# Kernel tuning notes

Measured on AMD Instinct MI355X. Metric: run time of the kernel, lower is better.

The kernel has to match this reference:

```python
import jax, jax.numpy as jnp
import numpy as np

B, M, C, IMG, P, D, L, H, DFF, NC = 16, 4, 3, 224, 16, 768, 12, 12, 3072, 1000
G = IMG // P
S = G * G + 1
HD = D // H
EPS = 1e-6
SCALE = HD ** -0.5


def setup_inputs() -> dict:
    key = jax.random.key(0)
    ks = jax.random.split(key, 12)
    w = lambda k, shape: (jax.random.normal(k, shape) * 0.02).astype(jnp.float32)
    return {
        'x': jax.random.normal(ks[0], (B, C, IMG, IMG), jnp.float32),
        'x_tangent': jax.random.normal(ks[1], (B, M, C, IMG, IMG), jnp.float32),
        'patch_w': w(ks[2], (D, C * P * P)), 'patch_b': jnp.zeros((D,), jnp.float32),
        'cls_token': w(ks[3], (1, 1, D)), 'pos_embed': w(ks[4], (1, S, D)),
        'ln1_g': jnp.ones((L, D), jnp.float32), 'ln1_b': jnp.zeros((L, D), jnp.float32),
        'qkv_w': w(ks[5], (L, 3 * D, D)), 'qkv_b': jnp.zeros((L, 3 * D), jnp.float32),
        'proj_w': w(ks[6], (L, D, D)), 'proj_b': jnp.zeros((L, D), jnp.float32),
        'ln2_g': jnp.ones((L, D), jnp.float32), 'ln2_b': jnp.zeros((L, D), jnp.float32),
        'fc1_w': w(ks[7], (L, DFF, D)), 'fc1_b': jnp.zeros((L, DFF), jnp.float32),
        'fc2_w': w(ks[8], (L, D, DFF)), 'fc2_b': jnp.zeros((L, D), jnp.float32),
        'normf_g': jnp.ones((D,), jnp.float32), 'normf_b': jnp.zeros((D,), jnp.float32),
        'head_w': w(ks[9], (NC, D)), 'head_b': jnp.zeros((NC,), jnp.float32),
    }


def _patchify(img):
    # [b,C,IMG,IMG] -> [b, G*G, C*P*P], matching Conv2d(patch) weight layout (c, ph, pw)
    b = img.shape[0]
    p = img.reshape(b, C, G, P, G, P).transpose(0, 2, 4, 1, 3, 5)
    return p.reshape(b, G * G, C * P * P)


def _ln_jvp(x, t, g, b):
    # x: [B,S,D], t: [B,M,S,D]; params constant w.r.t. tangent directions
    mu = x.mean(-1, keepdims=True)
    xc = x - mu
    inv = jax.lax.rsqrt((xc * xc).mean(-1, keepdims=True) + EPS)
    xh = xc * inv
    y = xh * g + b
    xh_b, inv_b = xh[:, None], inv[:, None]
    ty = g * inv_b * (t - t.mean(-1, keepdims=True) - xh_b * (xh_b * t).mean(-1, keepdims=True))
    return y, ty


def _gelu_jvp(x, t):
    # exact (erf) GELU and its derivative; x: [B,S,F], t: [B,M,S,F]
    cdf = 0.5 * (1.0 + jax.lax.erf(x * 0.7071067811865476))
    pdf = jnp.exp(-0.5 * x * x) * 0.3989422804014327
    return x * cdf, t * (cdf + x * pdf)[:, None]


def _softmax_jvp(s, ts):
    # s: [B,H,S,S], ts: [B,M,H,S,S]
    a = jax.nn.softmax(s, axis=-1)
    a_b = a[:, None]
    ta = a_b * (ts - (a_b * ts).sum(-1, keepdims=True))
    return a, ta


def reference(x, x_tangent, patch_w, patch_b, cls_token, pos_embed,
              ln1_g, ln1_b, qkv_w, qkv_b, proj_w, proj_b, ln2_g, ln2_b,
              fc1_w, fc1_b, fc2_w, fc2_b, normf_g, normf_b, head_w, head_b):
    # patch embed (primal + tangent; bias/pos/cls are constants -> zero tangent)
    h = _patchify(x) @ patch_w.T + patch_b                                  # [B,N,D]
    th = (_patchify(x_tangent.reshape(B * M, C, IMG, IMG)) @ patch_w.T).reshape(B, M, G * G, D)
    cls = jnp.broadcast_to(cls_token, (B, 1, D))
    h = jnp.concatenate([cls, h], axis=1) + pos_embed                       # [B,S,D]
    th = jnp.concatenate([jnp.zeros((B, M, 1, D), th.dtype), th], axis=2)   # [B,M,S,D]

    for l in range(L):
        # --- attention (manual JVP, matching the torch einsum path) ---
        y, ty = _ln_jvp(h, th, ln1_g[l], ln1_b[l])
        qkv = y @ qkv_w[l].T + qkv_b[l]
        tqkv = ty @ qkv_w[l].T
        q, k, v = jnp.split(qkv, 3, axis=-1)
        tq, tk, tv = jnp.split(tqkv, 3, axis=-1)
        q = q.reshape(B, S, H, HD); k = k.reshape(B, S, H, HD); v = v.reshape(B, S, H, HD)
        tq = tq.reshape(B, M, S, H, HD); tk = tk.reshape(B, M, S, H, HD); tv = tv.reshape(B, M, S, H, HD)
        s = jnp.einsum('bqhd,bkhd->bhqk', q, k) * SCALE
        ts = (jnp.einsum('bmqhd,bkhd->bmhqk', tq, k)
              + jnp.einsum('bqhd,bmkhd->bmhqk', q, tk)) * SCALE
        a, ta = _softmax_jvp(s, ts)
        o = jnp.einsum('bhqk,bkhd->bqhd', a, v).reshape(B, S, D)
        to = (jnp.einsum('bmhqk,bkhd->bmqhd', ta, v)
              + jnp.einsum('bhqk,bmkhd->bmqhd', a, tv)).reshape(B, M, S, D)
        h = h + o @ proj_w[l].T + proj_b[l]
        th = th + to @ proj_w[l].T
        # --- mlp ---
        y, ty = _ln_jvp(h, th, ln2_g[l], ln2_b[l])
        y = y @ fc1_w[l].T + fc1_b[l]
        ty = ty @ fc1_w[l].T
        y, ty = _gelu_jvp(y, ty)
        h = h + y @ fc2_w[l].T + fc2_b[l]
        th = th + ty @ fc2_w[l].T

    y, ty = _ln_jvp(h, th, normf_g, normf_b)
    logits = y[:, 0] @ head_w.T + head_b            # token pooling
    tlogits = ty[:, :, 0] @ head_w.T                 # [B,M,NC]
    return logits, tlogits
```

## Files before the change

kernel.cpp:

```cpp
#include <hip/hip_runtime.h>
#include <hip/hip_bf16.h>

#define DEVI __device__ __forceinline__

typedef short  bf16x8 __attribute__((ext_vector_type(8)));
typedef float  f32x4  __attribute__((ext_vector_type(4)));

static constexpr int BB   = 16;
static constexpr int MM   = 4;
static constexpr int CC   = 3;
static constexpr int IMG  = 224;
static constexpr int PPP  = 16;
static constexpr int DD   = 768;
static constexpr int LL   = 12;
static constexpr int HH   = 12;
static constexpr int DFF  = 3072;
static constexpr int NCLS = 1000;
static constexpr int GG   = 14;
static constexpr int SS   = 197;
static constexpr int HD   = 64;
static constexpr int BT   = BB*SS;
static constexpr int BMT  = BB*MM*SS;
static constexpr int RT   = BT+BMT;
static constexpr int RP   = 15872;
static constexpr int SP   = 208;
static constexpr int LDP  = 216;
static constexpr int QLD  = 3*DD;
static constexpr int PRP  = BB*GG*GG;
static constexpr int PRT  = (BB+BB*MM)*GG*GG;
static constexpr float EPSV  = 1e-6f;
static constexpr float SCALE = 0.125f;

static constexpr int NQW  = QLD*DD;
static constexpr int NPW  = DD*DD;
static constexpr int NF1W = DFF*DD;
static constexpr int NF2W = DD*DFF;
static constexpr int WTOT = NQW+NPW+NF1W+NF2W;

DEVI unsigned short f2bf(float x){
  union { float f; unsigned u; } v; v.f = x;
  unsigned r = v.u + 0x7fffu + ((v.u>>16)&1u);
  return (unsigned short)(r>>16);
}
DEVI float bf2f(unsigned short x){
  union { unsigned u; float f; } v; v.u = ((unsigned)x)<<16;
  return v.f;
}
DEVI f32x4 mfma16(bf16x8 a, bf16x8 b, f32x4 c){
  return __builtin_amdgcn_mfma_f32_16x16x32_bf16(a,b,c,0,0,0);
}
typedef const void __attribute__((address_space(1)))* gas1;
typedef void __attribute__((address_space(3)))* las3;


DEVI bf16x8 cvt8(const float* src){
  float4 a = *(const float4*)src;
  float4 b = *(const float4*)(src+4);
  bf16x8 o;
  o[0]=(short)f2bf(a.x); o[1]=(short)f2bf(a.y); o[2]=(short)f2bf(a.z); o[3]=(short)f2bf(a.w);
  o[4]=(short)f2bf(b.x); o[5]=(short)f2bf(b.y); o[6]=(short)f2bf(b.z); o[7]=(short)f2bf(b.w);
  return o;
}

__global__ __launch_bounds__(256) void f2bf8_kernel(const float* __restrict__ in,
    unsigned short* __restrict__ out, size_t n8){
  size_t i = (size_t)blockIdx.x*256 + threadIdx.x;
  if (i < n8) *(bf16x8*)(out + i*8) = cvt8(in + i*8);
}

__global__ __launch_bounds__(256) void conv_all_v(const float* __restrict__ qkvw,
    const float* __restrict__ projw, const float* __restrict__ f1w,
    const float* __restrict__ f2w, unsigned short* __restrict__ wl){
  int l = blockIdx.y;
  size_t i = ((size_t)blockIdx.x*256 + threadIdx.x)*8;
  const float* src;
  if (i < NQW)                src = qkvw + (size_t)l*NQW + i;
  else if (i < NQW+NPW)       src = projw + (size_t)l*NPW + (i-NQW);
  else if (i < NQW+NPW+NF1W)  src = f1w + (size_t)l*NF1W + (i-NQW-NPW);
  else                        src = f2w + (size_t)l*NF2W + (i-NQW-NPW-NF1W);
  *(bf16x8*)(wl + (size_t)l*WTOT + i) = cvt8(src);
}

__global__ __launch_bounds__(256) void conv_layer_v(const float* __restrict__ qkvw,
    const float* __restrict__ projw, const float* __restrict__ f1w,
    const float* __restrict__ f2w, unsigned short* __restrict__ wl){
  size_t i = ((size_t)blockIdx.x*256 + threadIdx.x)*8;
  const float* src;
  if (i < NQW)                src = qkvw + i;
  else if (i < NQW+NPW)       src = projw + (i-NQW);
  else if (i < NQW+NPW+NF1W)  src = f1w + (i-NQW-NPW);
  else                        src = f2w + (i-NQW-NPW-NF1W);
  *(bf16x8*)(wl + i) = cvt8(src);
}

__global__ __launch_bounds__(256) void init_h(float* __restrict__ hh,
    const float* __restrict__ cls, const float* __restrict__ pos,
    const float* __restrict__ patch_b){
  size_t i = (size_t)blockIdx.x*256 + threadIdx.x;
  int r = (int)(i/DD), c = (int)(i%DD);
  float v = 0.f;
  if (r < BT){
    int s_ = r % SS;
    v = pos[(size_t)s_*DD + c] + (s_==0 ? cls[c] : patch_b[c]);
  }
  hh[i] = v;
}

__global__ __launch_bounds__(256) void patchify_k(const float* __restrict__ x,
    const float* __restrict__ xt, unsigned short* __restrict__ pat){
  size_t i = (size_t)blockIdx.x*256 + threadIdx.x;
  int r = (int)(i/DD), kk = (int)(i%DD);
  int c = kk>>8, rem = kk&255, py = rem>>4, px = rem&15;
  const float* src;
  if (r < PRP){
    int b_ = r/(GG*GG), p = r%(GG*GG);
    src = x + (((size_t)b_*CC + c)*IMG + (size_t)(p/GG)*PPP + py)*IMG + (p%GG)*PPP + px;
  } else {
    int rr = r-PRP; int bm = rr/(GG*GG), p = rr%(GG*GG);
    src = xt + (((size_t)bm*CC + c)*IMG + (size_t)(p/GG)*PPP + py)*IMG + (p%GG)*PPP + px;
  }
  pat[i] = f2bf(*src);
}


DEVI void blockSum4(float&a,float&b,float&c,float&d,float* red){
  #pragma unroll
  for (int off=32; off; off>>=1){
    a += __shfl_xor(a,off,64); b += __shfl_xor(b,off,64);
    c += __shfl_xor(c,off,64); d += __shfl_xor(d,off,64);
  }
  int w = threadIdx.x>>6;
  if ((threadIdx.x&63)==0){ red[w]=a; red[4+w]=b; red[8+w]=c; red[12+w]=d; }
  __syncthreads();
  a = red[0]+red[1]+red[2]+red[3];
  b = red[4]+red[5]+red[6]+red[7];
  c = red[8]+red[9]+red[10]+red[11];
  d = red[12]+red[13]+red[14]+red[15];
  __syncthreads();
}

__global__ __launch_bounds__(256) void ln_group(const float* __restrict__ hh,
    const float* __restrict__ g, const float* __restrict__ bb,
    unsigned short* __restrict__ ybf){
  __shared__ float red[4][10];
  int r = blockIdx.x;
  int b_ = r/SS, s_ = r%SS;
  int t = threadIdx.x;
  const float* xx = hh + (size_t)r*DD;
  float x0=xx[t], x1=xx[t+256], x2=xx[t+512];
  size_t trow[4];
  float tv[4][3];
  #pragma unroll
  for (int m=0;m<4;m++){
    trow[m] = (size_t)BT + ((size_t)(b_*MM+m))*SS + s_;
    const float* tt = hh + trow[m]*DD;
    tv[m][0]=tt[t]; tv[m][1]=tt[t+256]; tv[m][2]=tt[t+512];
  }
  float s[10];
  s[0]=x0+x1+x2; s[1]=x0*x0+x1*x1+x2*x2;
  #pragma unroll
  for (int m=0;m<4;m++){
    s[2+2*m]=tv[m][0]+tv[m][1]+tv[m][2];
    s[3+2*m]=x0*tv[m][0]+x1*tv[m][1]+x2*tv[m][2];
  }
  #pragma unroll
  for (int k=0;k<10;k++){
    float v = s[k];
    #pragma unroll
    for (int off=32; off; off>>=1) v += __shfl_xor(v, off, 64);
    s[k] = v;
  }
  int w = t>>6;
  if ((t&63)==0){
    #pragma unroll
    for (int k=0;k<10;k++) red[w][k]=s[k];
  }
  __syncthreads();
  #pragma unroll
  for (int k=0;k<10;k++) s[k] = red[0][k]+red[1][k]+red[2][k]+red[3][k];
  float mu  = s[0]*(1.f/DD);
  float inv = rsqrtf(s[1]*(1.f/DD) - mu*mu + EPSV);
  float g0=g[t], g1=g[t+256], g2=g[t+512];
  float h0=(x0-mu)*inv, h1=(x1-mu)*inv, h2=(x2-mu)*inv;
  {
    unsigned short* y = ybf + (size_t)r*DD;
    y[t]     = f2bf(h0*g0 + bb[t]);
    y[t+256] = f2bf(h1*g1 + bb[t+256]);
    y[t+512] = f2bf(h2*g2 + bb[t+512]);
  }
  #pragma unroll
  for (int m=0;m<4;m++){
    float tmean = s[2+2*m]*(1.f/DD);
    float dot   = inv*(s[3+2*m]*(1.f/DD) - mu*tmean);
    unsigned short* y = ybf + trow[m]*DD;
    y[t]     = f2bf(g0*inv*(tv[m][0] - tmean - h0*dot));
    y[t+256] = f2bf(g1*inv*(tv[m][1] - tmean - h1*dot));
    y[t+512] = f2bf(g2*inv*(tv[m][2] - tmean - h2*dot));
  }
}

__global__ __launch_bounds__(256) void ln_head(const float* __restrict__ hh,
    const float* __restrict__ g, const float* __restrict__ bb,
    unsigned short* __restrict__ ybf){
  __shared__ float red[16];
  int ri = blockIdx.x;
  int t = threadIdx.x;
  if (ri < BB){
    size_t row = (size_t)ri*SS;
    const float* x = hh + row*DD;
    float x0=x[t], x1=x[t+256], x2=x[t+512];
    float s1=x0+x1+x2, s2=x0*x0+x1*x1+x2*x2, s3=0.f, s4=0.f;
    blockSum4(s1,s2,s3,s4,red);
    float mu  = s1*(1.f/DD);
    float inv = rsqrtf(s2*(1.f/DD) - mu*mu + EPSV);
    unsigned short* y = ybf + row*DD;
    y[t]     = f2bf((x0-mu)*inv*g[t]     + bb[t]);
    y[t+256] = f2bf((x1-mu)*inv*g[t+256] + bb[t+256]);
    y[t+512] = f2bf((x2-mu)*inv*g[t+512] + bb[t+512]);
  } else {
    int t2 = ri - BB;
    size_t row = (size_t)BT + (size_t)t2*SS;
    size_t prow = (size_t)(t2/MM)*SS;
    const float* tt = hh + row*DD;
    const float* xx = hh + prow*DD;
    float t0=tt[t], t1=tt[t+256], t2v=tt[t+512];
    float x0=xx[t], x1=xx[t+256], x2=xx[t+512];
    float s1=x0+x1+x2, s2=x0*x0+x1*x1+x2*x2;
    float s3=t0+t1+t2v, s4=x0*t0+x1*t1+x2*t2v;
    blockSum4(s1,s2,s3,s4,red);
    float mu  = s1*(1.f/DD);
    float inv = rsqrtf(s2*(1.f/DD) - mu*mu + EPSV);
    float tmean = s3*(1.f/DD);
    float dot   = inv*(s4*(1.f/DD) - mu*tmean);
    unsigned short* y = ybf + row*DD;
    y[t]     = f2bf(g[t]    *inv*(t0  - tmean - (x0-mu)*inv*dot));
    y[t+256] = f2bf(g[t+256]*inv*(t1  - tmean - (x1-mu)*inv*dot));
    y[t+512] = f2bf(g[t+512]*inv*(t2v - tmean - (x2-mu)*inv*dot));
  }
}


template<int MODE>
__global__ __launch_bounds__(256,2) void gemm_bt(
    const unsigned short* __restrict__ A,
    const unsigned short* __restrict__ Aalt, int asplit, int lda,
    const unsigned short* __restrict__ W, int K, int N, int Mrows,
    float* __restrict__ outf, unsigned short* __restrict__ outb, int ldc,
    const float* __restrict__ bias, int bias_limit)
{
  __shared__ __attribute__((aligned(16))) unsigned short As[128*64];
  __shared__ __attribute__((aligned(16))) unsigned short Bs[128*64];
  const int tid = threadIdx.x;
  const int wave = tid>>6, lane = tid&63;
  const int tM = blockIdx.y, tN = blockIdx.x;
  f32x4 acc[4][4];
  f32x4 zf = {0.f,0.f,0.f,0.f};
  #pragma unroll
  for (int m=0;m<4;m++)
    #pragma unroll
    for (int n=0;n<4;n++) acc[m][n] = zf;
  const int wm = wave>>1, wn = wave&1;
  const int lrow = lane&15, lk8 = (lane>>4)<<3;
  const int srow = tid>>3;
  const int scol = (tid&7)<<3;
  const size_t arow0 = (size_t)tM*128;
  const size_t brow0 = (size_t)tN*128;

  for (int k0=0; k0<K; k0+=64){
    #pragma unroll
    for (int i=0;i<4;i++){
      int row = (int)arow0 + srow + i*32;
      const unsigned short* abase = (row < asplit) ? Aalt : A;
      const unsigned short* ga = abase + (size_t)row*lda + (k0+scol);
      __builtin_amdgcn_global_load_lds((gas1)ga, (las3)(As + i*2048 + wave*512), 16, 0, 0);
      const unsigned short* gb = W + (brow0+srow+i*32)*(size_t)K + (k0+scol);
      __builtin_amdgcn_global_load_lds((gas1)gb, (las3)(Bs + i*2048 + wave*512), 16, 0, 0);
    }
    __syncthreads();
    #pragma unroll
    for (int kk=0; kk<64; kk+=32){
      bf16x8 af[4], bw[4];
      #pragma unroll
      for (int m=0;m<4;m++) af[m] = *(const bf16x8*)(As + (wm*64+m*16+lrow)*64 + kk+lk8);
      #pragma unroll
      for (int n=0;n<4;n++) bw[n] = *(const bf16x8*)(Bs + (wn*64+n*16+lrow)*64 + kk+lk8);
      #pragma unroll
      for (int m=0;m<4;m++)
        #pragma unroll
        for (int n=0;n<4;n++)
          acc[m][n] = mfma16(af[m], bw[n], acc[m][n]);
    }
    __syncthreads();
  }

  const int colbase = tN*128 + wn*64 + lrow;
  const int rowbase = tM*128 + wm*64 + ((lane>>4)<<2);
  #pragma unroll
  for (int n=0;n<4;n++){
    int col = colbase + n*16;
    #pragma unroll
    for (int m=0;m<4;m++){
      #pragma unroll
      for (int i=0;i<4;i++){
        int r = rowbase + m*16 + i;
        float v = acc[m][n][i];
        if (MODE==0){
          if (r < bias_limit) v += bias[col];
          outb[(size_t)r*ldc + col] = f2bf(v);
        } else if (MODE==1){
          if (r < Mrows){
            if (r < bias_limit) v += bias[col];
            outf[(size_t)r*ldc + col] += v;
          }
        } else {
          if (r < PRT){
            int orow;
            if (r < PRP) orow = (r/196)*197 + 1 + r%196;
            else { int rr = r-PRP; orow = BT + (rr/196)*197 + 1 + rr%196; }
            outf[(size_t)orow*ldc + col] += v;
          }
        }
      }
    }
  }
}

__global__ __launch_bounds__(256) void transpose_v(const unsigned short* __restrict__ qkv,
    unsigned short* __restrict__ vT, unsigned short* __restrict__ tvT){
  __shared__ unsigned short tile[SP*65];
  int inst = blockIdx.x;
  size_t rowbase; unsigned short* dst; int h;
  if (inst < BB*HH){ int b_=inst/HH; h=inst%HH; rowbase=(size_t)b_*SS; dst = vT + (size_t)inst*HD*SP; }
  else { int i2=inst-BB*HH; int bm=i2/HH; h=i2%HH; rowbase=(size_t)BT+(size_t)bm*SS; dst = tvT + (size_t)i2*HD*SP; }
  int coff = 2*DD + h*HD;
  for (int i=threadIdx.x; i<SP*HD; i+=256){
    int k = i>>6, d = i&63;
    unsigned short v = (k<SS) ? qkv[(rowbase+k)*QLD + coff + d] : (unsigned short)0;
    tile[k*65+d] = v;
  }
  __syncthreads();
  for (int i=threadIdx.x; i<HD*SP; i+=256){
    int d = i/SP, k = i%SP;
    dst[(size_t)d*SP + k] = tile[k*65+d];
  }
}

__global__ __launch_bounds__(256) void attn_s1_pv(const unsigned short* __restrict__ qkv,
    unsigned short* __restrict__ abf, const unsigned short* __restrict__ vT,
    unsigned short* __restrict__ obf){
  __shared__ __attribute__((aligned(16))) unsigned short pa[64*LDP];
  int qt = blockIdx.x, inst = blockIdx.y;
  int wave = threadIdx.x>>6, lane = threadIdx.x&63;
  int lrow = lane&15, lk = (lane>>4)<<3;
  int q0 = qt*64 + wave*16;
  f32x4 acc[13];
  f32x4 zf = {0.f,0.f,0.f,0.f};
  #pragma unroll
  for (int n=0;n<13;n++) acc[n]=zf;
  int h = inst % HH, b_ = inst / HH;
  size_t prow = (size_t)b_*SS;
  const unsigned short* Ab = qkv + (prow + q0 + lrow)*QLD + h*HD + lk;
  const unsigned short* Bb = qkv + prow*QLD + DD + h*HD + lk;
  #pragma unroll
  for (int kk=0; kk<HD; kk+=32){
    bf16x8 av = *(const bf16x8*)(Ab + kk);
    #pragma unroll
    for (int n=0;n<13;n++){
      bf16x8 bv = *(const bf16x8*)(Bb + (size_t)(n*16+lrow)*QLD + kk);
      acc[n] = mfma16(av, bv, acc[n]);
    }
  }
  int grp = lane>>4;
  unsigned short* obase = abf + (size_t)inst*SP*SP;
  bool okc12 = (lrow < 5);
  #pragma unroll
  for (int i=0;i<4;i++){
    int qr = q0 + grp*4 + i;
    float val[13], e[13];
    float mv = -1e30f;
    #pragma unroll
    for (int n=0;n<13;n++){
      val[n] = acc[n][i]*SCALE;
      if (n<12 || okc12) mv = fmaxf(mv, val[n]);
    }
    #pragma unroll
    for (int off=8; off; off>>=1) mv = fmaxf(mv, __shfl_xor(mv, off, 64));
    float s = 0.f;
    #pragma unroll
    for (int n=0;n<13;n++){
      e[n] = (n<12 || okc12) ? __expf(val[n]-mv) : 0.f;
      s += e[n];
    }
    #pragma unroll
    for (int off=8; off; off>>=1) s += __shfl_xor(s, off, 64);
    float inv = 1.f/s;
    unsigned short* lrp = pa + (size_t)(wave*16 + grp*4 + i)*LDP;
    unsigned short* orow = obase + (size_t)qr*SP;
    #pragma unroll
    for (int n=0;n<13;n++){
      unsigned short pv_ = f2bf(e[n]*inv);
      lrp[n*16+lrow] = pv_;
      if (qr < SS) orow[n*16+lrow] = pv_;
    }
  }
  __syncthreads();
  f32x4 pacc[4];
  #pragma unroll
  for (int n=0;n<4;n++) pacc[n]=zf;
  const unsigned short* Vb = vT + (size_t)inst*HD*SP;
  const unsigned short* Arow = pa + (size_t)(wave*16 + lrow)*LDP;
  #pragma unroll
  for (int ks=0; ks<6; ks++){
    int kb = ks*32 + lk;
    bf16x8 av = *(const bf16x8*)(Arow + kb);
    #pragma unroll
    for (int n=0;n<4;n++){
      bf16x8 bv = *(const bf16x8*)(Vb + (size_t)(n*16+lrow)*SP + kb);
      pacc[n] = mfma16(av, bv, pacc[n]);
    }
  }
  {
    int kb = 192 + lk;
    const bf16x8 ZV = {0,0,0,0,0,0,0,0};
    bool ok = (lk < 16);
    bf16x8 av = ok ? *(const bf16x8*)(Arow + kb) : ZV;
    #pragma unroll
    for (int n=0;n<4;n++){
      bf16x8 bv = ok ? *(const bf16x8*)(Vb + (size_t)(n*16+lrow)*SP + kb) : ZV;
      pacc[n] = mfma16(av, bv, pacc[n]);
    }
  }
  size_t orow0 = (size_t)b_*SS;
  int qr0 = q0 + (grp<<2);
  #pragma unroll
  for (int n=0;n<4;n++){
    int cc = h*HD + n*16 + lrow;
    #pragma unroll
    for (int i=0;i<4;i++){
      int qr = qr0 + i;
      if (qr < SS) obf[(orow0+qr)*DD + cc] = f2bf(pacc[n][i]);
    }
  }
}

__global__ __launch_bounds__(256) void attn_s2_pv(const unsigned short* __restrict__ qkv,
    const unsigned short* __restrict__ abf, const unsigned short* __restrict__ vT,
    const unsigned short* __restrict__ tvT, unsigned short* __restrict__ obf){
  __shared__ __attribute__((aligned(16))) unsigned short sa[64*LDP];
  __shared__ __attribute__((aligned(16))) unsigned short ta[64*LDP];
  int qt = blockIdx.x, il = blockIdx.y;
  int wave = threadIdx.x>>6, lane = threadIdx.x&63;
  int lrow = lane&15, lk = (lane>>4)<<3;
  int q0 = qt*64 + wave*16;
  int h = il % HH;
  int bmix = il / HH;
  int b_ = bmix / MM;
  int bh = b_*HH + h;
  {
    const unsigned short* abase = abf + (size_t)bh*SP*SP;
    int qb = qt*64;
    for (int c = threadIdx.x; c < 64*26; c += 256){
      int rl = c/26, c8 = (c%26)*8;
      int qr = qb + rl; if (qr > SS-1) qr = SS-1;
      *(bf16x8*)(sa + (size_t)rl*LDP + c8) = *(const bf16x8*)(abase + (size_t)qr*SP + c8);
    }
  }
  f32x4 acc[13];
  f32x4 zf = {0.f,0.f,0.f,0.f};
  #pragma unroll
  for (int n=0;n<13;n++) acc[n]=zf;
  size_t prow = (size_t)b_*SS;
  size_t trow = (size_t)BT + (size_t)bmix*SS;
  #pragma unroll
  for (int p=0;p<2;p++){
    size_t ar = (p==0) ? trow : prow;
    size_t br = (p==1) ? trow : prow;
    const unsigned short* Ab = qkv + (ar + q0 + lrow)*QLD + h*HD + lk;
    const unsigned short* Bb = qkv + br*QLD + DD + h*HD + lk;
    #pragma unroll
    for (int kk=0; kk<HD; kk+=32){
      bf16x8 av = *(const bf16x8*)(Ab + kk);
      #pragma unroll
      for (int n=0;n<13;n++){
        bf16x8 bv = *(const bf16x8*)(Bb + (size_t)(n*16+lrow)*QLD + kk);
        acc[n] = mfma16(av, bv, acc[n]);
      }
    }
  }
  __syncthreads();
  int grp = lane>>4;
  #pragma unroll
  for (int i=0;i<4;i++){
    int rl = wave*16 + grp*4 + i;
    const unsigned short* arow = sa + (size_t)rl*LDP;
    float av[13], tv[13];
    float dot = 0.f;
    #pragma unroll
    for (int n=0;n<13;n++){
      tv[n] = acc[n][i]*SCALE;
      av[n] = bf2f(arow[n*16+lrow]);
      dot += av[n]*tv[n];
    }
    #pragma unroll
    for (int off=8; off; off>>=1) dot += __shfl_xor(dot, off, 64);
    unsigned short* trp = ta + (size_t)rl*LDP;
    #pragma unroll
    for (int n=0;n<13;n++) trp[n*16+lrow] = f2bf(av[n]*(tv[n]-dot));
  }
  __syncthreads();
  f32x4 pacc[4];
  #pragma unroll
  for (int n=0;n<4;n++) pacc[n]=zf;
  #pragma unroll
  for (int p=0;p<2;p++){
    const unsigned short* Arow = (p==0 ? ta : sa) + (size_t)(wave*16 + lrow)*LDP;
    const unsigned short* Bb = (p==0) ? vT + (size_t)bh*HD*SP
                                      : tvT + (size_t)il*HD*SP;
    #pragma unroll
    for (int ks=0; ks<6; ks++){
      int kb = ks*32 + lk;
      bf16x8 av = *(const bf16x8*)(Arow + kb);
      #pragma unroll
      for (int n=0;n<4;n++){
        bf16x8 bv = *(const bf16x8*)(Bb + (size_t)(n*16+lrow)*SP + kb);
        pacc[n] = mfma16(av, bv, pacc[n]);
      }
    }
    {
      int kb = 192 + lk;
      const bf16x8 ZV = {0,0,0,0,0,0,0,0};
      bool ok = (lk < 16);
      bf16x8 av = ok ? *(const bf16x8*)(Arow + kb) : ZV;
      #pragma unroll
      for (int n=0;n<4;n++){
        bf16x8 bv = ok ? *(const bf16x8*)(Bb + (size_t)(n*16+lrow)*SP + kb) : ZV;
        pacc[n] = mfma16(av, bv, pacc[n]);
      }
    }
  }
  size_t orow0 = (size_t)BT + (size_t)bmix*SS;
  int qr0 = q0 + (grp<<2);
  #pragma unroll
  for (int n=0;n<4;n++){
    int cc = h*HD + n*16 + lrow;
    #pragma unroll
    for (int i=0;i<4;i++){
      int qr = qr0 + i;
      if (qr < SS) obf[(orow0+qr)*DD + cc] = f2bf(pacc[n][i]);
    }
  }
}

__global__ __launch_bounds__(256) void gelu_group(unsigned short* __restrict__ fc1o,
                                                  unsigned short* __restrict__ pgbf){
  int r = blockIdx.x;
  int b_ = r/SS, s_ = r%SS;
  const bf16x8* pb = (const bf16x8*)(fc1o + (size_t)r*DFF);
  bf16x8* pg = (bf16x8*)(pgbf + (size_t)r*DFF);
  bf16x8* tb[4];
  #pragma unroll
  for (int m=0;m<4;m++)
    tb[m] = (bf16x8*)(fc1o + ((size_t)BT + (size_t)(b_*MM+m)*SS + s_)*DFF);
  for (int c = threadIdx.x; c < DFF/8; c += 256){
    bf16x8 xv = pb[c];
    float deriv[8];
    bf16x8 o;
    #pragma unroll
    for (int j=0;j<8;j++){
      float x = bf2f((unsigned short)xv[j]);
      float cdf = 0.5f*(1.f + erff(x*0.70710678118654752f));
      float pdf = __expf(-0.5f*x*x)*0.39894228040143267f;
      o[j] = (short)f2bf(x*cdf);
      deriv[j] = cdf + x*pdf;
    }
    pg[c] = o;
    #pragma unroll
    for (int m=0;m<4;m++){
      bf16x8 tv8 = tb[m][c];
      bf16x8 w;
      #pragma unroll
      for (int j=0;j<8;j++) w[j] = (short)f2bf(bf2f((unsigned short)tv8[j])*deriv[j]);
      tb[m][c] = w;
    }
  }
}

__global__ __launch_bounds__(256) void head_k(const unsigned short* __restrict__ ybf,
    const float* __restrict__ hw, const float* __restrict__ hb, float* __restrict__ out){
  __shared__ float ysh[DD];
  int ri = blockIdx.x;
  size_t yrow; float* o; bool wb;
  if (ri < BB){ yrow = (size_t)ri*SS; o = out + (size_t)ri*NCLS; wb = true; }
  else { int t2 = ri-BB; yrow = (size_t)BT + (size_t)t2*SS; o = out + (size_t)BB*NCLS + (size_t)t2*NCLS; wb = false; }
  for (int d=threadIdx.x; d<DD; d+=256) ysh[d] = bf2f(ybf[yrow*DD + d]);
  __syncthreads();
  for (int n=threadIdx.x; n<NCLS; n+=256){
    const float* wrow = hw + (size_t)n*DD;
    float acc = wb ? hb[n] : 0.f;
    for (int d=0; d<DD; d++) acc += ysh[d]*wrow[d];
    o[n] = acc;
  }
}

extern "C" void kernel_launch(void* const* d_in, const int* in_sizes, int n_in,
                              void* d_out, int out_size, void* d_ws, size_t ws_size,
                              hipStream_t stream)
{
  const float* x      = (const float*)d_in[0];
  const float* xt     = (const float*)d_in[1];
  const float* patch_w= (const float*)d_in[2];
  const float* patch_b= (const float*)d_in[3];
  const float* cls    = (const float*)d_in[4];
  const float* pos    = (const float*)d_in[5];
  const float* ln1_g  = (const float*)d_in[6];
  const float* ln1_b  = (const float*)d_in[7];
  const float* qkv_w  = (const float*)d_in[8];
  const float* qkv_b  = (const float*)d_in[9];
  const float* proj_w = (const float*)d_in[10];
  const float* proj_b = (const float*)d_in[11];
  const float* ln2_g  = (const float*)d_in[12];
  const float* ln2_b  = (const float*)d_in[13];
  const float* fc1_w  = (const float*)d_in[14];
  const float* fc1_b  = (const float*)d_in[15];
  const float* fc2_w  = (const float*)d_in[16];
  const float* fc2_b  = (const float*)d_in[17];
  const float* nf_g   = (const float*)d_in[18];
  const float* nf_b   = (const float*)d_in[19];
  const float* head_w = (const float*)d_in[20];
  const float* head_b = (const float*)d_in[21];
  float* out = (float*)d_out;

  char* ws = (char*)d_ws;
  size_t off = 0;
  auto alloc = [&](size_t bytes)->char*{
    char* p = ws + off;
    off = (off + bytes + 255) & ~(size_t)255;
    return p;
  };

  unsigned short *w_patch, *wl, *ybf, *qkvbf, *vT, *tvT, *abf, *fc1o, *pgbf;
  float *hh;
  auto layout = [&](bool allw)->size_t{
    off = 0;
    w_patch = (unsigned short*)alloc((size_t)DD*DD*2);
    wl      = (unsigned short*)alloc((size_t)WTOT*2*(allw?LL:1));
    hh      = (float*)alloc((size_t)RP*DD*4);
    ybf     = (unsigned short*)alloc((size_t)RP*DD*2);
    size_t slab0 = off;
    qkvbf = (unsigned short*)alloc((size_t)RP*QLD*2);
    vT    = (unsigned short*)alloc((size_t)BB*HH*HD*SP*2);
    tvT   = (unsigned short*)alloc((size_t)BB*MM*HH*HD*SP*2);
    abf   = (unsigned short*)alloc((size_t)BB*HH*SP*SP*2);
    size_t endA = off;
    off = slab0;
    fc1o = (unsigned short*)alloc((size_t)RP*DFF*2);
    pgbf = (unsigned short*)alloc((size_t)BT*DFF*2);
    size_t endB = off;
    return (endA > endB) ? endA : endB;
  };

  bool allw = true;
  size_t need = layout(true);
  if (need > ws_size){ need = layout(false); allw = false; }
  if (need > ws_size){
    (void)hipMemsetAsync(d_out, 0x7f, (size_t)out_size*4, stream);
    return;
  }

  dim3 blk(256);
  f2bf8_kernel<<<dim3((DD*DD/8+255)/256), blk, 0, stream>>>(patch_w, w_patch, (size_t)DD*DD/8);
  if (allw)
    conv_all_v<<<dim3(WTOT/8/256, LL), blk, 0, stream>>>(qkv_w, proj_w, fc1_w, fc2_w, wl);
  init_h<<<dim3((RP*DD)/256), blk, 0, stream>>>(hh, cls, pos, patch_b);
  patchify_k<<<dim3((PRT*DD)/256), blk, 0, stream>>>(x, xt, ybf);
  gemm_bt<2><<<dim3(DD/128, 123), blk, 0, stream>>>(ybf, nullptr, 0, DD, w_patch, DD, DD, PRT,
                                                    hh, nullptr, DD, nullptr, 0);

  for (int l=0; l<LL; l++){
    if (!allw)
      conv_layer_v<<<dim3(WTOT/8/256), blk, 0, stream>>>(qkv_w+(size_t)l*NQW, proj_w+(size_t)l*NPW,
                                                         fc1_w+(size_t)l*NF1W, fc2_w+(size_t)l*NF2W, wl);
    const unsigned short* w_qkv = wl + (allw ? (size_t)l*WTOT : 0);
    const unsigned short* w_proj= w_qkv + NQW;
    const unsigned short* w_fc1 = w_qkv + NQW + NPW;
    const unsigned short* w_fc2 = w_qkv + NQW + NPW + NF1W;

    ln_group<<<dim3(BT), blk, 0, stream>>>(hh, ln1_g+(size_t)l*DD, ln1_b+(size_t)l*DD, ybf);
    gemm_bt<0><<<dim3(QLD/128, RP/128), blk, 0, stream>>>(ybf, nullptr, 0, DD, w_qkv,
        DD, QLD, RT, nullptr, qkvbf, QLD, qkv_b+(size_t)l*QLD, BT);
    transpose_v<<<dim3(BB*HH + BB*MM*HH), blk, 0, stream>>>(qkvbf, vT, tvT);
    attn_s1_pv<<<dim3(4, BB*HH), blk, 0, stream>>>(qkvbf, abf, vT, ybf);
    attn_s2_pv<<<dim3(4, BB*MM*HH), blk, 0, stream>>>(qkvbf, abf, vT, tvT, ybf);
    gemm_bt<1><<<dim3(DD/128, RP/128), blk, 0, stream>>>(ybf, nullptr, 0, DD, w_proj,
        DD, DD, RT, hh, nullptr, DD, proj_b+(size_t)l*DD, BT);
    ln_group<<<dim3(BT), blk, 0, stream>>>(hh, ln2_g+(size_t)l*DD, ln2_b+(size_t)l*DD, ybf);
    gemm_bt<0><<<dim3(DFF/128, RP/128), blk, 0, stream>>>(ybf, nullptr, 0, DD, w_fc1,
        DD, DFF, RT, nullptr, fc1o, DFF, fc1_b+(size_t)l*DFF, BT);
    gelu_group<<<dim3(BT), blk, 0, stream>>>(fc1o, pgbf);
    gemm_bt<1><<<dim3(DD/128, RP/128), blk, 0, stream>>>(fc1o, pgbf, BT, DFF, w_fc2,
        DFF, DD, RT, hh, nullptr, DD, fc2_b+(size_t)l*DD, BT);
  }

  ln_head<<<dim3(BB + BB*MM), blk, 0, stream>>>(hh, nf_g, nf_b, ybf);
  head_k<<<dim3(BB + BB*MM), blk, 0, stream>>>(ybf, head_w, head_b, out);
}
```

Baseline: 7.476 ms.

## Use 256x256 double-buffered GEMM with swizzled LDS and 8 waves

Replaces the 128x128 single-buffered bf16 GEMM with a 256x256 tile kernel using 512 threads (8 waves, each computing 128x64). It double-buffers the LDS stages so the next K-tile's global-to-LDS load overlaps the current MFMAs, and removes one barrier per iteration. It also XOR-swizzles the LDS column slots to avoid bank conflicts and raises wave priority around the MFMA block. The larger tile cuts operand re-fetch per FLOP. The cost is 128KB of LDS per block, which may allow only one block per CU, plus fewer blocks overall (e.g. 3x62 for the D-wide GEMMs) and higher register pressure from 32 accumulators.

Measured after the change: 9.096 ms. 1.22x slower.

```diff
diff --git a/kernel.cpp b/kernel.cpp
--- a/kernel.cpp
+++ b/kernel.cpp
@@ -241,65 +241,100 @@
 
 
 template<int MODE>
-__global__ __launch_bounds__(256,2) void gemm_bt(
+__global__ __launch_bounds__(512,2) void gemm_bt8(
     const unsigned short* __restrict__ A,
     const unsigned short* __restrict__ Aalt, int asplit, int lda,
     const unsigned short* __restrict__ W, int K, int N, int Mrows,
     float* __restrict__ outf, unsigned short* __restrict__ outb, int ldc,
     const float* __restrict__ bias, int bias_limit)
 {
-  __shared__ __attribute__((aligned(16))) unsigned short As[128*64];
-  __shared__ __attribute__((aligned(16))) unsigned short Bs[128*64];
+  __shared__ __attribute__((aligned(16))) unsigned short As[2][256*64];
+  __shared__ __attribute__((aligned(16))) unsigned short Bs[2][256*64];
   const int tid = threadIdx.x;
-  const int wave = tid>>6, lane = tid&63;
+  const int lane = tid&63;
+  const int wave = tid>>6;
   const int tM = blockIdx.y, tN = blockIdx.x;
-  f32x4 acc[4][4];
+  const int wm = wave>>2, wn = wave&3;
+  const int lrow = lane&15;
+  const int lslot = lane>>4;
+  const int srow8 = tid>>3;
+  const int sslot = tid&7;
+
+  f32x4 acc[8][4];
   f32x4 zf = {0.f,0.f,0.f,0.f};
   #pragma unroll
-  for (int m=0;m<4;m++)
+  for (int m=0;m<8;m++)
     #pragma unroll
     for (int n=0;n<4;n++) acc[m][n] = zf;
-  const int wm = wave>>1, wn = wave&1;
-  const int lrow = lane&15, lk8 = (lane>>4)<<3;
-  const int srow = tid>>3;
-  const int scol = (tid&7)<<3;
-  const size_t arow0 = (size_t)tM*128;
-  const size_t brow0 = (size_t)tN*128;
-
-  for (int k0=0; k0<K; k0+=64){
-    #pragma unroll
-    for (int i=0;i<4;i++){
-      int row = (int)arow0 + srow + i*32;
-      const unsigned short* abase = (row < asplit) ? Aalt : A;
-      const unsigned short* ga = abase + (size_t)row*lda + (k0+scol);
-      __builtin_amdgcn_global_load_lds((gas1)ga, (las3)(As + i*2048 + wave*512), 16, 0, 0);
-      const unsigned short* gb = W + (brow0+srow+i*32)*(size_t)K + (k0+scol);
-      __builtin_amdgcn_global_load_lds((gas1)gb, (las3)(Bs + i*2048 + wave*512), 16, 0, 0);
+
+  const int nk = K>>6;
+
+  auto stage = [&](int kt, int b){
+    const int k0 = kt<<6;
+    #pragma unroll
+    for (int c=0;c<4;c++){
+      int rD = c*64 + srow8;
+      int gcol = k0 + ((sslot ^ (rD&7))<<3);
+      int grow = tM*256 + rD;
+      const unsigned short* ab = (grow < asplit) ? Aalt : A;
+      __builtin_amdgcn_global_load_lds((gas1)(ab + (size_t)grow*lda + gcol),
+          (las3)(As[b] + c*4096 + tid*8), 16, 0, 0);
+      const unsigned short* gb = W + (size_t)(tN*256 + rD)*K + gcol;
+      __builtin_amdgcn_global_load_lds((gas1)gb,
+          (las3)(Bs[b] + c*4096 + tid*8), 16, 0, 0);
+    }
+  };
+
+  stage(0, 0);
+  __syncthreads();
+  int buf = 0;
+  for (int t=0; t<nk; ++t){
+    if (t+1 < nk) stage(t+1, buf^1);
+    #pragma unroll
+    for (int mh=0; mh<2; ++mh){
+      #pragma unroll
+      for (int nh=0; nh<2; ++nh){
+        bf16x8 af[4][2], bw[2][2];
+        #pragma unroll
+        for (int mi=0; mi<4; ++mi){
+          int r = wm*128 + (mh*4+mi)*16 + lrow;
+          #pragma unroll
+          for (int kk=0; kk<2; ++kk){
+            int cs = kk*4 + lslot;
+            af[mi][kk] = *(const bf16x8*)(As[buf] + r*64 + ((cs ^ (r&7))<<3));
+          }
+        }
+        #pragma unroll
+        for (int ni=0; ni<2; ++ni){
+          int r = wn*64 + (nh*2+ni)*16 + lrow;
+          #pragma unroll
+          for (int kk=0; kk<2; ++kk){
+            int cs = kk*4 + lslot;
+            bw[ni][kk] = *(const bf16x8*)(Bs[buf] + r*64 + ((cs ^ (r&7))<<3));
+          }
+        }
+        __builtin_amdgcn_s_setprio(1);
+        #pragma unroll
+        for (int mi=0; mi<4; ++mi)
+          #pragma unroll
+          for (int ni=0; ni<2; ++ni)
+            #pragma unroll
+            for (int kk=0; kk<2; ++kk)
+              acc[mh*4+mi][nh*2+ni] = mfma16(af[mi][kk], bw[ni][kk], acc[mh*4+mi][nh*2+ni]);
+        __builtin_amdgcn_s_setprio(0);
+      }
     }
     __syncthreads();
-    #pragma unroll
-    for (int kk=0; kk<64; kk+=32){
-      bf16x8 af[4], bw[4];
-      #pragma unroll
-      for (int m=0;m<4;m++) af[m] = *(const bf16x8*)(As + (wm*64+m*16+lrow)*64 + kk+lk8);
-      #pragma unroll
-      for (int n=0;n<4;n++) bw[n] = *(const bf16x8*)(Bs + (wn*64+n*16+lrow)*64 + kk+lk8);
-      #pragma unroll
-      for (int m=0;m<4;m++)
-        #pragma unroll
-        for (int n=0;n<4;n++)
-          acc[m][n] = mfma16(af[m], bw[n], acc[m][n]);
-    }
-    __syncthreads();
-  }
-
-  const int colbase = tN*128 + wn*64 + lrow;
-  const int rowbase = tM*128 + wm*64 + ((lane>>4)<<2);
+    buf ^= 1;
+  }
+
+  const int colbase = tN*256 + wn*64 + lrow;
+  const int rowbase = tM*256 + wm*128 + ((lane>>4)<<2);
   #pragma unroll
   for (int n=0;n<4;n++){
     int col = colbase + n*16;
     #pragma unroll
-    for (int m=0;m<4;m++){
+    for (int m=0;m<8;m++){
       #pragma unroll
       for (int i=0;i<4;i++){
         int r = rowbase + m*16 + i;
@@ -668,13 +703,14 @@
   }
 
   dim3 blk(256);
+  dim3 gblk(512);
   f2bf8_kernel<<<dim3((DD*DD/8+255)/256), blk, 0, stream>>>(patch_w, w_patch, (size_t)DD*DD/8);
   if (allw)
     conv_all_v<<<dim3(WTOT/8/256, LL), blk, 0, stream>>>(qkv_w, proj_w, fc1_w, fc2_w, wl);
   init_h<<<dim3((RP*DD)/256), blk, 0, stream>>>(hh, cls, pos, patch_b);
   patchify_k<<<dim3((PRT*DD)/256), blk, 0, stream>>>(x, xt, ybf);
-  gemm_bt<2><<<dim3(DD/128, 123), blk, 0, stream>>>(ybf, nullptr, 0, DD, w_patch, DD, DD, PRT,
-                                                    hh, nullptr, DD, nullptr, 0);
+  gemm_bt8<2><<<dim3(DD/256, RP/256), gblk, 0, stream>>>(ybf, nullptr, 0, DD, w_patch, DD, DD, PRT,
+                                                         hh, nullptr, DD, nullptr, 0);
 
   for (int l=0; l<LL; l++){
     if (!allw)
@@ -686,18 +722,18 @@
     const unsigned short* w_fc2 = w_qkv + NQW + NPW + NF1W;
 
     ln_group<<<dim3(BT), blk, 0, stream>>>(hh, ln1_g+(size_t)l*DD, ln1_b+(size_t)l*DD, ybf);
-    gemm_bt<0><<<dim3(QLD/128, RP/128), blk, 0, stream>>>(ybf, nullptr, 0, DD, w_qkv,
+    gemm_bt8<0><<<dim3(QLD/256, RP/256), gblk, 0, stream>>>(ybf, nullptr, 0, DD, w_qkv,
         DD, QLD, RT, nullptr, qkvbf, QLD, qkv_b+(size_t)l*QLD, BT);
     transpose_v<<<dim3(BB*HH + BB*MM*HH), blk, 0, stream>>>(qkvbf, vT, tvT);
     attn_s1_pv<<<dim3(4, BB*HH), blk, 0, stream>>>(qkvbf, abf, vT, ybf);
     attn_s2_pv<<<dim3(4, BB*MM*HH), blk, 0, stream>>>(qkvbf, abf, vT, tvT, ybf);
-    gemm_bt<1><<<dim3(DD/128, RP/128), blk, 0, stream>>>(ybf, nullptr, 0, DD, w_proj,
+    gemm_bt8<1><<<dim3(DD/256, RP/256), gblk, 0, stream>>>(ybf, nullptr, 0, DD, w_proj,
         DD, DD, RT, hh, nullptr, DD, proj_b+(size_t)l*DD, BT);
     ln_group<<<dim3(BT), blk, 0, stream>>>(hh, ln2_g+(size_t)l*DD, ln2_b+(size_t)l*DD, ybf);
-    gemm_bt<0><<<dim3(DFF/128, RP/128), blk, 0, stream>>>(ybf, nullptr, 0, DD, w_fc1,
+    gemm_bt8<0><<<dim3(DFF/256, RP/256), gblk, 0, stream>>>(ybf, nullptr, 0, DD, w_fc1,
         DD, DFF, RT, nullptr, fc1o, DFF, fc1_b+(size_t)l*DFF, BT);
     gelu_group<<<dim3(BT), blk, 0, stream>>>(fc1o, pgbf);
-    gemm_bt<1><<<dim3(DD/128, RP/128), blk, 0, stream>>>(fc1o, pgbf, BT, DFF, w_fc2,
+    gemm_bt8<1><<<dim3(DD/256, RP/256), gblk, 0, stream>>>(fc1o, pgbf, BT, DFF, w_fc2,
         DFF, DD, RT, hh, nullptr, DD, fc2_b+(size_t)l*DD, BT);
   }
 
```
